# Performance work log

Measured on AMD Instinct MI355X. Metric: run time of the kernel, lower is better.

Reference implementation:

```python
import jax, jax.numpy as jnp
import numpy as np

B, D, H, W, C = 2, 128, 128, 128, 8
GD = GH = GW = 96


def setup_inputs() -> dict:
    key = jax.random.key(0)
    k1, k2 = jax.random.split(key)
    inputs = jax.random.normal(k1, (B, D, H, W, C), dtype=jnp.float32)
    # sample_coords uniform over the valid voxel range [0, size-1] per spatial dim
    sizes = jnp.array([D - 1, H - 1, W - 1], dtype=jnp.float32)
    sample_coords = jax.random.uniform(k2, (B, GD, GH, GW, 3), dtype=jnp.float32) * sizes
    return {"inputs": inputs, "sample_coords": sample_coords}


def reference(inputs, sample_coords):
    # Trilinear resampling with REPLICATE boundary (clamp), matching
    # ResamplerLayer.resample_linear + boundary_replicate.
    input_size = inputs.shape[1:-1]                       # (D, H, W)
    rank = len(input_size)                                # 3
    floor_c = jnp.floor(sample_coords)                    # [B, gd, gh, gw, 3]
    w = sample_coords - floor_c                           # fractional weights
    wc = 1.0 - w
    i0 = floor_c.astype(jnp.int32)
    c0 = [jnp.clip(i0[..., d], 0, input_size[d] - 1) for d in range(rank)]
    c1 = [jnp.clip(i0[..., d] + 1, 0, input_size[d] - 1) for d in range(rank)]

    bsz = sample_coords.shape[0]
    batch_idx = jnp.arange(bsz).reshape((bsz,) + (1,) * (sample_coords.ndim - 2))

    # Sum over the 2^rank corners; identical math to the recursive
    # pyramid_combination in the original (fixed small unrolled loop).
    out = jnp.zeros(sample_coords.shape[:-1] + (inputs.shape[-1],), inputs.dtype)
    for code in range(2 ** rank):
        bits = [(code >> (rank - 1 - d)) & 1 for d in range(rank)]
        idx = [c1[d] if bits[d] else c0[d] for d in range(rank)]
        samp = inputs[batch_idx, idx[0], idx[1], idx[2]]  # [B, gd, gh, gw, C]
        wt = jnp.ones(sample_coords.shape[:-1], inputs.dtype)
        for d in range(rank):
            wt = wt * (w[..., d] if bits[d] else wc[..., d])
        out = out + samp * wt[..., None]
    return out
```

## Files before the change

### kernel.cpp

```cpp
#include <hip/hip_runtime.h>
#include <stdint.h>


constexpr int B  = 2;
constexpr int D  = 128;
constexpr int H  = 128;
constexpr int W  = 128;
constexpr int C  = 8;
constexpr int GD = 96;
constexpr int GH = 96;
constexpr int GW = 96;
constexpr long long PTS_PER_B = (long long)GD * GH * GW;
constexpr long long NPTS      = (long long)B * PTS_PER_B;
constexpr int NPTS_I = (int)NPTS;

constexpr int TPZ = 16, TPY = 16, TPX = 16;
constexpr int NT_PER_B = TPZ * TPY * TPX;
constexpr int NT = B * NT_PER_B;

constexpr int RZ = 9, RY = 9, RX = 9;
constexpr int RVOX = RZ * RY * RX;

constexpr int TPB_BIN = 1024;
constexpr int PPT     = 8;
constexpr int NB_BIN  = NPTS_I / (TPB_BIN * PPT);
static_assert(NB_BIN * TPB_BIN * PPT == NPTS_I, "exact tiling");
constexpr int BPT = NT / TPB_BIN;

constexpr int BUCKETS_PER_BLOCK = 4;
constexpr int NBLK4 = NT / BUCKETS_PER_BLOCK;

__device__ __forceinline__ int clampi(int v, int lo, int hi) {
    return min(max(v, lo), hi);
}

__device__ __forceinline__ int tile_of(int b, float zc, float yc, float xc) {
    int z0 = clampi((int)floorf(zc), 0, D - 1);
    int y0 = clampi((int)floorf(yc), 0, H - 1);
    int x0 = clampi((int)floorf(xc), 0, W - 1);
    return (b << 12) | ((z0 >> 3) << 8) | ((y0 >> 3) << 4) | (x0 >> 3);
}

__device__ __forceinline__ unsigned long long
pack_rec(int i, float zc, float yc, float xc, int b, int& tk)
{
    const int z0 = clampi((int)floorf(zc), 0, D - 1);
    const int y0 = clampi((int)floorf(yc), 0, H - 1);
    const int x0 = clampi((int)floorf(xc), 0, W - 1);
    const int tz = z0 >> 3, ty = y0 >> 3, tx = x0 >> 3;
    tk = (b << 12) | (tz << 8) | (ty << 4) | tx;
    const int qz = clampi((int)((zc - (float)(tz << 3)) * 1024.0f + 0.5f), 0, 8191);
    const int qy = clampi((int)((yc - (float)(ty << 3)) * 1024.0f + 0.5f), 0, 8191);
    const int qx = clampi((int)((xc - (float)(tx << 3)) * 1024.0f + 0.5f), 0, 8191);
    return (unsigned long long)(uint32_t)i
         | ((unsigned long long)qx << 21)
         | ((unsigned long long)qy << 34)
         | ((unsigned long long)qz << 47);
}

__device__ __forceinline__ uint32_t bf16_rne(float f) {
    uint32_t u = __float_as_uint(f);
    u += 0x7FFFu + ((u >> 16) & 1u);
    return u >> 16;
}
__device__ __forceinline__ uint32_t pack_bf16(float lo, float hi) {
    return bf16_rne(lo) | (bf16_rne(hi) << 16);
}

__global__ __launch_bounds__(TPB_BIN)
void k_hist(const float* __restrict__ coords, uint16_t* __restrict__ blockHist)
{
    __shared__ uint32_t h[NT];
    const int t = threadIdx.x;
#pragma unroll
    for (int j = 0; j < BPT; ++j) h[t + j * TPB_BIN] = 0u;
    __syncthreads();

    const int base = blockIdx.x * (TPB_BIN * PPT);
#pragma unroll
    for (int k = 0; k < PPT; ++k) {
        const int i = base + k * TPB_BIN + t;
        const float zc = coords[3 * i + 0];
        const float yc = coords[3 * i + 1];
        const float xc = coords[3 * i + 2];
        const int b = (i >= (int)PTS_PER_B) ? 1 : 0;
        atomicAdd(&h[tile_of(b, zc, yc, xc)], 1u);
    }
    __syncthreads();
#pragma unroll
    for (int j = 0; j < BPT; ++j) {
        const int c = t + j * TPB_BIN;
        blockHist[blockIdx.x * NT + c] = (uint16_t)h[c];
    }
}

__global__ __launch_bounds__(128)
void k_scan_cols(uint16_t* __restrict__ blockHist, uint32_t* __restrict__ bucketTot)
{
    const int c = blockIdx.x * 128 + threadIdx.x;
    uint32_t acc = 0u;
#pragma unroll 8
    for (int r = 0; r < NB_BIN; ++r) {
        const int o = r * NT + c;
        const uint32_t v = blockHist[o];
        blockHist[o] = (uint16_t)acc;
        acc += v;
    }
    bucketTot[c] = acc;
}

__global__ __launch_bounds__(TPB_BIN)
void k_scan_base(const uint32_t* __restrict__ bucketTot, uint32_t* __restrict__ bucketBase)
{
    __shared__ uint32_t ss[TPB_BIN];
    const int t = threadIdx.x;

    uint32_t l[BPT];
    uint32_t ls = 0u;
#pragma unroll
    for (int j = 0; j < BPT; ++j) {
        l[j] = bucketTot[t * BPT + j];
        ls += l[j];
    }
    ss[t] = ls;
    __syncthreads();
    for (int off = 1; off < TPB_BIN; off <<= 1) {
        const uint32_t v = (t >= off) ? ss[t - off] : 0u;
        __syncthreads();
        ss[t] += v;
        __syncthreads();
    }
    uint32_t basev = ss[t] - ls;
#pragma unroll
    for (int j = 0; j < BPT; ++j) {
        bucketBase[t * BPT + j] = basev;
        basev += l[j];
    }
    if (t == TPB_BIN - 1) bucketBase[NT] = (uint32_t)NPTS_I;
}

__global__ __launch_bounds__(TPB_BIN)
void k_scatter(const float* __restrict__ coords,
               const uint16_t* __restrict__ blockHist,
               const uint32_t* __restrict__ bucketBase,
               unsigned long long* __restrict__ records)
{
    __shared__ uint32_t cur[NT];
    const int t = threadIdx.x;
#pragma unroll
    for (int j = 0; j < BPT; ++j) {
        const int c = t + j * TPB_BIN;
        cur[c] = (uint32_t)blockHist[blockIdx.x * NT + c] + bucketBase[c];
    }
    __syncthreads();

    const int base = blockIdx.x * (TPB_BIN * PPT);
#pragma unroll
    for (int k = 0; k < PPT; ++k) {
        const int i = base + k * TPB_BIN + t;
        const float zc = coords[3 * i + 0];
        const float yc = coords[3 * i + 1];
        const float xc = coords[3 * i + 2];
        const int b = (i >= (int)PTS_PER_B) ? 1 : 0;
        int tk;
        const unsigned long long r = pack_rec(i, zc, yc, xc, b, tk);
        const uint32_t slot = atomicAdd(&cur[tk], 1u);
        records[slot] = r;
    }
}

__device__ __forceinline__ void
process_rec(unsigned long long r, const uint4* __restrict__ tb,
            float* __restrict__ out)
{
    const int idx = (int)(r & 0x1FFFFFull);
    const int qx  = (int)((r >> 21) & 0x1FFFull);
    const int qy  = (int)((r >> 34) & 0x1FFFull);
    const int qz  = (int)((r >> 47) & 0x1FFFull);
    const int lx = qx >> 10, ly = qy >> 10, lz = qz >> 10;
    const float wx1 = (float)(qx & 1023) * (1.0f / 1024.0f), wx0 = 1.0f - wx1;
    const float wy1 = (float)(qy & 1023) * (1.0f / 1024.0f), wy0 = 1.0f - wy1;
    const float wz1 = (float)(qz & 1023) * (1.0f / 1024.0f), wz0 = 1.0f - wz1;

    const int vi = (lz * RY + ly) * RX + lx;

    float a0 = 0.f, a1 = 0.f, a2 = 0.f, a3 = 0.f;
    float a4 = 0.f, a5 = 0.f, a6 = 0.f, a7 = 0.f;
    const float wzs[2] = {wz0, wz1};
    const float wys[2] = {wy0, wy1};
    const float wxs[2] = {wx0, wx1};

#pragma unroll
    for (int iz = 0; iz < 2; ++iz) {
#pragma unroll
        for (int iy = 0; iy < 2; ++iy) {
#pragma unroll
            for (int ix = 0; ix < 2; ++ix) {
                const float wt = wzs[iz] * wys[iy] * wxs[ix];
                const int cv = vi + (iz * RY + iy) * RX + ix;
                const uint4 rv = tb[cv];
                a0 += wt * __uint_as_float(rv.x << 16);
                a1 += wt * __uint_as_float(rv.x & 0xFFFF0000u);
                a2 += wt * __uint_as_float(rv.y << 16);
                a3 += wt * __uint_as_float(rv.y & 0xFFFF0000u);
                a4 += wt * __uint_as_float(rv.z << 16);
                a5 += wt * __uint_as_float(rv.z & 0xFFFF0000u);
                a6 += wt * __uint_as_float(rv.w << 16);
                a7 += wt * __uint_as_float(rv.w & 0xFFFF0000u);
            }
        }
    }

    float* o = out + (long long)idx * C;
    *reinterpret_cast<float4*>(o)     = make_float4(a0, a1, a2, a3);
    *reinterpret_cast<float4*>(o + 4) = make_float4(a4, a5, a6, a7);
}

__global__ __launch_bounds__(256)
void k_sample_tiled(const float* __restrict__ inp,
                    const unsigned long long* __restrict__ records,
                    const uint32_t* __restrict__ bucketBase,
                    float* __restrict__ out)
{
    __shared__ uint4 tile[2][RVOX];
    const int t = threadIdx.x;

    const int gb = ((int)blockIdx.x & 7) * (NBLK4 >> 3) + ((int)blockIdx.x >> 3);
    const int c0 = gb * BUCKETS_PER_BLOCK;

    float4 pv0[3], pv1[3];
    unsigned long long pr = 0ull;
    bool pr_valid = false;

    auto issue_voxels = [&](int c) {
        const int tx = c & 15, ty = (c >> 4) & 15, tz = (c >> 8) & 15, b = c >> 12;
        const int z0r = tz << 3, y0r = ty << 3, x0r = tx << 3;
#pragma unroll
        for (int j = 0; j < 3; ++j) {
            const int v = t + j * 256;
            if (v < RVOX) {
                const int lz = v / (RY * RX);
                const int rr = v - lz * (RY * RX);
                const int ly = rr / RX;
                const int lx = rr - ly * RX;
                const int gz = min(z0r + lz, D - 1);
                const int gy = min(y0r + ly, H - 1);
                const int gx = min(x0r + lx, W - 1);
                const int a = ((((b << 7) | gz) << 7 | gy) << 7 | gx) * C;
                pv0[j] = *reinterpret_cast<const float4*>(inp + a);
                pv1[j] = *reinterpret_cast<const float4*>(inp + a + 4);
            }
        }
    };
    auto issue_rec = [&](int c) {
        const uint32_t s = bucketBase[c];
        const uint32_t e = bucketBase[c + 1];
        const uint32_t i = s + (uint32_t)t;
        pr_valid = (i < e);
        if (pr_valid) pr = records[i];
    };

    issue_voxels(c0);
    issue_rec(c0);

    for (int k = 0; k < BUCKETS_PER_BLOCK; ++k) {
        const int c = c0 + k;
        uint4* tb = tile[k & 1];

#pragma unroll
        for (int j = 0; j < 3; ++j) {
            const int v = t + j * 256;
            if (v < RVOX) {
                uint4 pk;
                pk.x = pack_bf16(pv0[j].x, pv0[j].y);
                pk.y = pack_bf16(pv0[j].z, pv0[j].w);
                pk.z = pack_bf16(pv1[j].x, pv1[j].y);
                pk.w = pack_bf16(pv1[j].z, pv1[j].w);
                tb[v] = pk;
            }
        }
        const uint32_t s = bucketBase[c];
        const uint32_t e = bucketBase[c + 1];
        const unsigned long long r0 = pr;
        const bool r0v = pr_valid;
        __syncthreads();

        if (k + 1 < BUCKETS_PER_BLOCK) { issue_voxels(c + 1); issue_rec(c + 1); }

        if (r0v) process_rec(r0, tb, out);
        for (uint32_t i = s + (uint32_t)t + 256u; i < e; i += 256u)
            process_rec(records[i], tb, out);
    }
}

__global__ __launch_bounds__(256)
void resample_direct(const float* __restrict__ inp,
                     const float* __restrict__ coords,
                     float* __restrict__ out)
{
    const long long i = (long long)blockIdx.x * blockDim.x + threadIdx.x;
    if (i >= NPTS) return;
    const int b = (i >= PTS_PER_B) ? 1 : 0;
    const float zc = coords[3 * i + 0];
    const float yc = coords[3 * i + 1];
    const float xc = coords[3 * i + 2];
    const float fz = floorf(zc), fy = floorf(yc), fx = floorf(xc);
    const float wz1 = zc - fz, wz0 = 1.0f - wz1;
    const float wy1 = yc - fy, wy0 = 1.0f - wy1;
    const float wx1 = xc - fx, wx0 = 1.0f - wx1;
    const int z0 = clampi((int)fz, 0, D - 1);
    const int y0 = clampi((int)fy, 0, H - 1);
    const int x0 = clampi((int)fx, 0, W - 1);
    const int z1 = min(z0 + 1, D - 1);
    const int y1 = min(y0 + 1, H - 1);
    const int x1 = min(x0 + 1, W - 1);
    float4 acc_lo = make_float4(0.f, 0.f, 0.f, 0.f);
    float4 acc_hi = make_float4(0.f, 0.f, 0.f, 0.f);
    const int   zs[2]  = {z0, z1};
    const int   ys[2]  = {y0, y1};
    const int   xs[2]  = {x0, x1};
    const float wzs[2] = {wz0, wz1};
    const float wys[2] = {wy0, wy1};
    const float wxs[2] = {wx0, wx1};
#pragma unroll
    for (int iz = 0; iz < 2; ++iz)
#pragma unroll
        for (int iy = 0; iy < 2; ++iy)
#pragma unroll
            for (int ix = 0; ix < 2; ++ix) {
                const float wt = wzs[iz] * wys[iy] * wxs[ix];
                const int base = ((((b << 7) | zs[iz]) << 7 | ys[iy]) << 7 | xs[ix]) * C;
                const float4 v0 = *reinterpret_cast<const float4*>(inp + base);
                const float4 v1 = *reinterpret_cast<const float4*>(inp + base + 4);
                acc_lo.x += wt * v0.x;  acc_lo.y += wt * v0.y;
                acc_lo.z += wt * v0.z;  acc_lo.w += wt * v0.w;
                acc_hi.x += wt * v1.x;  acc_hi.y += wt * v1.y;
                acc_hi.z += wt * v1.z;  acc_hi.w += wt * v1.w;
            }
    float* o = out + i * C;
    *reinterpret_cast<float4*>(o)     = acc_lo;
    *reinterpret_cast<float4*>(o + 4) = acc_hi;
}

extern "C" void kernel_launch(void* const* d_in, const int* in_sizes, int n_in,
                              void* d_out, int out_size, void* d_ws, size_t ws_size,
                              hipStream_t stream)
{
    const float* inp    = (const float*)d_in[0];
    const float* coords = (const float*)d_in[1];
    float* out          = (float*)d_out;

    const size_t rec_bytes  = (size_t)NPTS_I * sizeof(unsigned long long);
    const size_t hist_bytes = (size_t)NB_BIN * NT * sizeof(uint16_t);
    const size_t base_bytes = (size_t)(NT + 1) * sizeof(uint32_t);
    const size_t tot_bytes  = (size_t)NT * sizeof(uint32_t);
    const size_t needed     = rec_bytes + hist_bytes + base_bytes + tot_bytes;

    if (ws_size < needed) {
        const int nblk = (NPTS_I + 255) / 256;
        resample_direct<<<nblk, 256, 0, stream>>>(inp, coords, out);
        return;
    }

    unsigned long long* records = (unsigned long long*)d_ws;
    uint16_t* blockHist  = (uint16_t*)((char*)d_ws + rec_bytes);
    uint32_t* bucketBase = (uint32_t*)((char*)d_ws + rec_bytes + hist_bytes);
    uint32_t* bucketTot  = (uint32_t*)((char*)d_ws + rec_bytes + hist_bytes + base_bytes);

    k_hist        <<<NB_BIN,   TPB_BIN, 0, stream>>>(coords, blockHist);
    k_scan_cols   <<<NT / 128, 128,     0, stream>>>(blockHist, bucketTot);
    k_scan_base   <<<1,        TPB_BIN, 0, stream>>>(bucketTot, bucketBase);
    k_scatter     <<<NB_BIN,   TPB_BIN, 0, stream>>>(coords, blockHist, bucketBase, records);
    k_sample_tiled<<<NBLK4,    256,     0, stream>>>(inp, records, bucketBase, out);
}
```

Baseline: 95.66 us.

## Widen bucket tiles along x and use one bucket per block

Bucket tiles become 8x8x16 voxels (halo 9x9x17) instead of 8x8x8, which halves the bucket count and cuts the redundant halo loads per sampled point. The sampling kernel drops the multi-bucket double-buffered prefetch loop and instead launches one block per bucket, loading the larger tile in two halves and prefetching two records per thread. The record packing changes to a 14-bit x offset. This trades the software pipelining inside a block for more blocks and less halo overhead, and uses a larger shared tile per block.

```diff
diff --git a/kernel.cpp b/kernel.cpp
--- a/kernel.cpp
+++ b/kernel.cpp
@@ -14,11 +14,11 @@
 constexpr long long NPTS      = (long long)B * PTS_PER_B;
 constexpr int NPTS_I = (int)NPTS;
 
-constexpr int TPZ = 16, TPY = 16, TPX = 16;
+constexpr int TPZ = 16, TPY = 16, TPX = 8;
 constexpr int NT_PER_B = TPZ * TPY * TPX;
 constexpr int NT = B * NT_PER_B;
 
-constexpr int RZ = 9, RY = 9, RX = 9;
+constexpr int RZ = 9, RY = 9, RX = 17;
 constexpr int RVOX = RZ * RY * RX;
 
 constexpr int TPB_BIN = 1024;
@@ -27,35 +27,32 @@
 static_assert(NB_BIN * TPB_BIN * PPT == NPTS_I, "exact tiling");
 constexpr int BPT = NT / TPB_BIN;
 
-constexpr int BUCKETS_PER_BLOCK = 4;
-constexpr int NBLK4 = NT / BUCKETS_PER_BLOCK;
-
 __device__ __forceinline__ int clampi(int v, int lo, int hi) {
     return min(max(v, lo), hi);
+}
+
+__device__ __forceinline__ unsigned long long
+pack_rec(int i, float zc, float yc, float xc, int b, int& tk)
+{
+    const int z0 = clampi((int)floorf(zc), 0, D - 1);
+    const int y0 = clampi((int)floorf(yc), 0, H - 1);
+    const int x0 = clampi((int)floorf(xc), 0, W - 1);
+    const int tz = z0 >> 3, ty = y0 >> 3, tx = x0 >> 4;
+    tk = (b << 11) | (tz << 7) | (ty << 3) | tx;
+    const int qz = clampi((int)((zc - (float)(tz << 3)) * 1024.0f + 0.5f), 0,  8191);
+    const int qy = clampi((int)((yc - (float)(ty << 3)) * 1024.0f + 0.5f), 0,  8191);
+    const int qx = clampi((int)((xc - (float)(tx << 4)) * 1024.0f + 0.5f), 0, 16383);
+    return (unsigned long long)(uint32_t)i
+         | ((unsigned long long)qx << 21)
+         | ((unsigned long long)qy << 35)
+         | ((unsigned long long)qz << 48);
 }
 
 __device__ __forceinline__ int tile_of(int b, float zc, float yc, float xc) {
     int z0 = clampi((int)floorf(zc), 0, D - 1);
     int y0 = clampi((int)floorf(yc), 0, H - 1);
     int x0 = clampi((int)floorf(xc), 0, W - 1);
-    return (b << 12) | ((z0 >> 3) << 8) | ((y0 >> 3) << 4) | (x0 >> 3);
-}
-
-__device__ __forceinline__ unsigned long long
-pack_rec(int i, float zc, float yc, float xc, int b, int& tk)
-{
-    const int z0 = clampi((int)floorf(zc), 0, D - 1);
-    const int y0 = clampi((int)floorf(yc), 0, H - 1);
-    const int x0 = clampi((int)floorf(xc), 0, W - 1);
-    const int tz = z0 >> 3, ty = y0 >> 3, tx = x0 >> 3;
-    tk = (b << 12) | (tz << 8) | (ty << 4) | tx;
-    const int qz = clampi((int)((zc - (float)(tz << 3)) * 1024.0f + 0.5f), 0, 8191);
-    const int qy = clampi((int)((yc - (float)(ty << 3)) * 1024.0f + 0.5f), 0, 8191);
-    const int qx = clampi((int)((xc - (float)(tx << 3)) * 1024.0f + 0.5f), 0, 8191);
-    return (unsigned long long)(uint32_t)i
-         | ((unsigned long long)qx << 21)
-         | ((unsigned long long)qy << 34)
-         | ((unsigned long long)qz << 47);
+    return (b << 11) | ((z0 >> 3) << 7) | ((y0 >> 3) << 3) | (x0 >> 4);
 }
 
 __device__ __forceinline__ uint32_t bf16_rne(float f) {
@@ -174,9 +171,9 @@
             float* __restrict__ out)
 {
     const int idx = (int)(r & 0x1FFFFFull);
-    const int qx  = (int)((r >> 21) & 0x1FFFull);
-    const int qy  = (int)((r >> 34) & 0x1FFFull);
-    const int qz  = (int)((r >> 47) & 0x1FFFull);
+    const int qx  = (int)((r >> 21) & 0x3FFFull);
+    const int qy  = (int)((r >> 35) & 0x1FFFull);
+    const int qz  = (int)((r >> 48) & 0x1FFFull);
     const int lx = qx >> 10, ly = qy >> 10, lz = qz >> 10;
     const float wx1 = (float)(qx & 1023) * (1.0f / 1024.0f), wx0 = 1.0f - wx1;
     const float wy1 = (float)(qy & 1023) * (1.0f / 1024.0f), wy0 = 1.0f - wy1;
@@ -222,22 +219,32 @@
                     const uint32_t* __restrict__ bucketBase,
                     float* __restrict__ out)
 {
-    __shared__ uint4 tile[2][RVOX];
+    __shared__ uint4 tile[RVOX];
     const int t = threadIdx.x;
 
-    const int gb = ((int)blockIdx.x & 7) * (NBLK4 >> 3) + ((int)blockIdx.x >> 3);
-    const int c0 = gb * BUCKETS_PER_BLOCK;
-
-    float4 pv0[3], pv1[3];
-    unsigned long long pr = 0ull;
-    bool pr_valid = false;
-
-    auto issue_voxels = [&](int c) {
-        const int tx = c & 15, ty = (c >> 4) & 15, tz = (c >> 8) & 15, b = c >> 12;
-        const int z0r = tz << 3, y0r = ty << 3, x0r = tx << 3;
+    const int g = blockIdx.x;
+    const int c = (g & 7) * (NT >> 3) + (g >> 3);
+
+    const int tx = c & 7;
+    const int ty = (c >> 3) & 15;
+    const int tz = (c >> 7) & 15;
+    const int b  = c >> 11;
+    const int z0r = tz << 3, y0r = ty << 3, x0r = tx << 4;
+
+    const uint32_t s = bucketBase[c];
+    const uint32_t e = bucketBase[c + 1];
+    const bool v0 = (s + (uint32_t)t        < e);
+    const bool v1 = (s + (uint32_t)t + 256u < e);
+    unsigned long long r0 = 0ull, r1 = 0ull;
+    if (v0) r0 = records[s + (uint32_t)t];
+    if (v1) r1 = records[s + (uint32_t)t + 256u];
+
+#pragma unroll
+    for (int half = 0; half < 2; ++half) {
+        float4 a0[3], a1[3];
 #pragma unroll
         for (int j = 0; j < 3; ++j) {
-            const int v = t + j * 256;
+            const int v = t + (half * 3 + j) * 256;
             if (v < RVOX) {
                 const int lz = v / (RY * RX);
                 const int rr = v - lz * (RY * RX);
@@ -247,50 +254,29 @@
                 const int gy = min(y0r + ly, H - 1);
                 const int gx = min(x0r + lx, W - 1);
                 const int a = ((((b << 7) | gz) << 7 | gy) << 7 | gx) * C;
-                pv0[j] = *reinterpret_cast<const float4*>(inp + a);
-                pv1[j] = *reinterpret_cast<const float4*>(inp + a + 4);
+                a0[j] = *reinterpret_cast<const float4*>(inp + a);
+                a1[j] = *reinterpret_cast<const float4*>(inp + a + 4);
             }
         }
-    };
-    auto issue_rec = [&](int c) {
-        const uint32_t s = bucketBase[c];
-        const uint32_t e = bucketBase[c + 1];
-        const uint32_t i = s + (uint32_t)t;
-        pr_valid = (i < e);
-        if (pr_valid) pr = records[i];
-    };
-
-    issue_voxels(c0);
-    issue_rec(c0);
-
-    for (int k = 0; k < BUCKETS_PER_BLOCK; ++k) {
-        const int c = c0 + k;
-        uint4* tb = tile[k & 1];
-
 #pragma unroll
         for (int j = 0; j < 3; ++j) {
-            const int v = t + j * 256;
+            const int v = t + (half * 3 + j) * 256;
             if (v < RVOX) {
                 uint4 pk;
-                pk.x = pack_bf16(pv0[j].x, pv0[j].y);
-                pk.y = pack_bf16(pv0[j].z, pv0[j].w);
-                pk.z = pack_bf16(pv1[j].x, pv1[j].y);
-                pk.w = pack_bf16(pv1[j].z, pv1[j].w);
-                tb[v] = pk;
+                pk.x = pack_bf16(a0[j].x, a0[j].y);
+                pk.y = pack_bf16(a0[j].z, a0[j].w);
+                pk.z = pack_bf16(a1[j].x, a1[j].y);
+                pk.w = pack_bf16(a1[j].z, a1[j].w);
+                tile[v] = pk;
             }
         }
-        const uint32_t s = bucketBase[c];
-        const uint32_t e = bucketBase[c + 1];
-        const unsigned long long r0 = pr;
-        const bool r0v = pr_valid;
-        __syncthreads();
-
-        if (k + 1 < BUCKETS_PER_BLOCK) { issue_voxels(c + 1); issue_rec(c + 1); }
-
-        if (r0v) process_rec(r0, tb, out);
-        for (uint32_t i = s + (uint32_t)t + 256u; i < e; i += 256u)
-            process_rec(records[i], tb, out);
-    }
+    }
+    __syncthreads();
+
+    if (v0) process_rec(r0, tile, out);
+    if (v1) process_rec(r1, tile, out);
+    for (uint32_t i = s + (uint32_t)t + 512u; i < e; i += 256u)
+        process_rec(records[i], tile, out);
 }
 
 __global__ __launch_bounds__(256)
@@ -371,5 +357,5 @@
     k_scan_cols   <<<NT / 128, 128,     0, stream>>>(blockHist, bucketTot);
     k_scan_base   <<<1,        TPB_BIN, 0, stream>>>(bucketTot, bucketBase);
     k_scatter     <<<NB_BIN,   TPB_BIN, 0, stream>>>(coords, blockHist, bucketBase, records);
-    k_sample_tiled<<<NBLK4,    256,     0, stream>>>(inp, records, bucketBase, out);
-}
+    k_sample_tiled<<<NT,       256,     0, stream>>>(inp, records, bucketBase, out);
+}
```

After: 86.96 us, median of 2. -9.1%, faster.
